# Kernel tuning notes

Measured on AMD Instinct MI355X. Metric: run time of the kernel, lower is better.

## Reference

```python
import jax, jax.numpy as jnp
import numpy as np

D_MODEL = 2048
N_HEADS = 16
HEAD_DIM = D_MODEL // N_HEADS
BATCH = 2
SEQ = 2048


def rotate_half(x):
    x1, x2 = jnp.split(x, 2, axis=-1)
    return jnp.concatenate((-x2, x1), axis=-1)


def rope_emb(seq_len, head_dim, dtype=jnp.float32):
    inv_freq = 1.0 / (10000.0 ** (jnp.arange(0, head_dim, 2, dtype=jnp.float32) / head_dim))
    t = jnp.arange(seq_len, dtype=jnp.float32)
    freqs = jnp.einsum('i,j->ij', t, inv_freq)            # [S, D/2]
    emb = jnp.concatenate((freqs, freqs), axis=-1)        # [S, D]
    return emb[None, :, None, :].astype(dtype)            # [1, S, 1, D]


def apply_rope(x, emb):
    return x * jnp.cos(emb) + rotate_half(x) * jnp.sin(emb)


def setup_inputs() -> dict:
    key = jax.random.key(0)
    ks = jax.random.split(key, 5)
    s = 1.0 / np.sqrt(D_MODEL)
    return {
        'query': jax.random.normal(ks[0], (BATCH, SEQ, D_MODEL), jnp.float32),
        'Wq': jax.random.normal(ks[1], (D_MODEL, D_MODEL), jnp.float32) * s,
        'Wk': jax.random.normal(ks[2], (D_MODEL, D_MODEL), jnp.float32) * s,
        'Wv': jax.random.normal(ks[3], (D_MODEL, D_MODEL), jnp.float32) * s,
        'Wo': jax.random.normal(ks[4], (D_MODEL, D_MODEL), jnp.float32) * s,
    }


def reference(query, Wq, Wk, Wv, Wo):
    B, S, _ = query.shape
    # QKV projections (nn.Linear: x @ W.T), reshape to [B, S, H, Dh]
    q = (query @ Wq.T).reshape(B, S, N_HEADS, HEAD_DIM)
    k = (query @ Wk.T).reshape(B, S, N_HEADS, HEAD_DIM)
    v = (query @ Wv.T).reshape(B, S, N_HEADS, HEAD_DIM)
    emb = rope_emb(S, HEAD_DIM, q.dtype)
    q = apply_rope(q, emb)
    k = apply_rope(k, emb)
    # causal SDPA
    scale = HEAD_DIM ** -0.5
    scores = jnp.einsum('bqhd,bkhd->bhqk', q, k) * scale  # [B, H, S, S]
    causal = jnp.tril(jnp.ones((S, S), dtype=bool))
    scores = jnp.where(causal, scores, jnp.finfo(scores.dtype).min)
    attn = jax.nn.softmax(scores, axis=-1)
    out = jnp.einsum('bhqk,bkhd->bqhd', attn, v).reshape(B, S, D_MODEL)
    return out @ Wo.T
```

## Files before the change

kernel.cpp:

```cpp
#include <hip/hip_runtime.h>
#include <math.h>

#define BATCH 2
#define SEQ 2048
#define DMODEL 2048
#define NHEADS 16
#define HEADDIM 128
#define MTOT (BATCH * SEQ)
#define QKVLD 6144

typedef __attribute__((ext_vector_type(8))) _Float16 half8;
typedef __attribute__((ext_vector_type(4))) _Float16 half4;
typedef __attribute__((ext_vector_type(4))) float f32x4;

__device__ __forceinline__ void gl_lds16(const void* g, void* l) {
    __builtin_amdgcn_global_load_lds(
        (const __attribute__((address_space(1))) unsigned int*)g,
        (__attribute__((address_space(3))) unsigned int*)l, 16, 0, 0);
}

__global__ __launch_bounds__(256) void f2h_multi(const float* __restrict__ query,
                                                 const float* __restrict__ Wq,
                                                 const float* __restrict__ Wk,
                                                 const float* __restrict__ Wv,
                                                 const float* __restrict__ Wo,
                                                 _Float16* __restrict__ xh,
                                                 _Float16* __restrict__ Wh3,
                                                 _Float16* __restrict__ woh) {
    const float* src;
    _Float16* dst;
    size_t i;
    int bx = blockIdx.x;
    if (bx < 4096) {
        src = query; dst = xh;
        i = ((size_t)bx * 256 + threadIdx.x) * 8;
    } else {
        int wi = bx - 4096;
        int y = wi >> 11;
        int off = wi & 2047;
        src = (y == 0) ? Wq : (y == 1) ? Wk : (y == 2) ? Wv : Wo;
        dst = (y == 3) ? woh : Wh3 + (size_t)y * (DMODEL * DMODEL);
        i = ((size_t)off * 256 + threadIdx.x) * 8;
    }
    float4 a = *(const float4*)(src + i);
    float4 b = *(const float4*)(src + i + 4);
    union { uint4 u; _Float16 h[8]; } o;
    o.h[0] = (_Float16)a.x; o.h[1] = (_Float16)a.y;
    o.h[2] = (_Float16)a.z; o.h[3] = (_Float16)a.w;
    o.h[4] = (_Float16)b.x; o.h[5] = (_Float16)b.y;
    o.h[6] = (_Float16)b.z; o.h[7] = (_Float16)b.w;
    *(uint4*)(dst + i) = o.u;
}

__global__ __launch_bounds__(256) void f2h_conv(const float* __restrict__ src,
                                                _Float16* __restrict__ dst) {
    size_t i = ((size_t)blockIdx.x * 256 + threadIdx.x) * 8;
    float4 a = *(const float4*)(src + i);
    float4 b = *(const float4*)(src + i + 4);
    union { uint4 u; _Float16 h[8]; } o;
    o.h[0] = (_Float16)a.x; o.h[1] = (_Float16)a.y;
    o.h[2] = (_Float16)a.z; o.h[3] = (_Float16)a.w;
    o.h[4] = (_Float16)b.x; o.h[5] = (_Float16)b.y;
    o.h[6] = (_Float16)b.z; o.h[7] = (_Float16)b.w;
    *(uint4*)(dst + i) = o.u;
}

#define SB0  __builtin_amdgcn_sched_barrier(0)
#define BAR  __builtin_amdgcn_s_barrier()
#define VMW4 do { SB0; asm volatile("s_waitcnt vmcnt(4)"); SB0; } while (0)
#define VMW0 do { SB0; asm volatile("s_waitcnt vmcnt(0)"); SB0; } while (0)

template <bool F16OUT>
__global__ __launch_bounds__(512, 2) void gemm8p(const _Float16* __restrict__ A,
                                                 const _Float16* __restrict__ W,
                                                 void* __restrict__ Cout,
                                                 int M, int N, int K) {
    __shared__ __align__(16) _Float16 LAb[2][2][128][64];
    __shared__ __align__(16) _Float16 LBb[2][2][128][64];

    const int tid = threadIdx.x;
    const int lane = tid & 63;
    const int wave = tid >> 6;
    const int quad = lane >> 4;
    const int lcol = lane & 15;
    const int wr = wave >> 2;
    const int wc = wave & 3;
    const int m0 = blockIdx.y * 256;
    const int n0 = blockIdx.x * 256;

    const int srow = tid >> 3;
    const int sc8p = tid & 7;
    const int sc8l = sc8p ^ (srow & 7);

#define STA(BUF, HALF, KT)                                                     \
    do {                                                                       \
        _Pragma("unroll") for (int j = 0; j < 2; j++)                          \
            gl_lds16(A + (size_t)(m0 + (HALF)*128 + j*64 + srow) * K +         \
                         (KT)*64 + sc8l*8,                                     \
                     &LAb[BUF][HALF][j*64 + srow][sc8p*8]);                    \
    } while (0)
#define STB(BUF, HALF, KT)                                                     \
    do {                                                                       \
        _Pragma("unroll") for (int j = 0; j < 2; j++)                          \
            gl_lds16(W + (size_t)(n0 + (HALF)*128 + j*64 + srow) * K +         \
                         (KT)*64 + sc8l*8,                                     \
                     &LBb[BUF][HALF][j*64 + srow][sc8p*8]);                    \
    } while (0)

    auto rdA = [&](int buf, int mf, int ks) -> half8 {
        int R = mf * 16 + lcol;
        return *(const half8*)&LAb[buf][wr][R]
                [(ks * 32 + quad * 8) ^ ((lcol & 7) << 3)];
    };
    auto rdB = [&](int buf, int nf, int ks) -> half8 {
        int R = (wc & 1) * 64 + nf * 16 + lcol;
        return *(const half8*)&LBb[buf][wc >> 1][R]
                [(ks * 32 + quad * 8) ^ ((lcol & 7) << 3)];
    };

    f32x4 acc[8][4];
#pragma unroll
    for (int i = 0; i < 8; i++)
#pragma unroll
        for (int j = 0; j < 4; j++) acc[i][j] = (f32x4){0.f, 0.f, 0.f, 0.f};

#define KTILE4(BUF, S1, S2, S3, S4, W4)                                        \
    {                                                                          \
        half8 a[4][2], b[4][2];                                                \
        _Pragma("unroll") for (int mf = 0; mf < 4; mf++)                       \
            _Pragma("unroll") for (int ks = 0; ks < 2; ks++)                   \
                a[mf][ks] = rdA(BUF, mf, ks);                                  \
        _Pragma("unroll") for (int nf = 0; nf < 2; nf++)                       \
            _Pragma("unroll") for (int ks = 0; ks < 2; ks++)                   \
                b[nf][ks] = rdB(BUF, nf, ks);                                  \
        S1; SB0; BAR; SB0;                                                     \
        __builtin_amdgcn_s_setprio(1);                                         \
        _Pragma("unroll") for (int ks = 0; ks < 2; ks++)                       \
            _Pragma("unroll") for (int mf = 0; mf < 4; mf++)                   \
                _Pragma("unroll") for (int nf = 0; nf < 2; nf++)               \
                    acc[mf][nf] = __builtin_amdgcn_mfma_f32_16x16x32_f16(      \
                        a[mf][ks], b[nf][ks], acc[mf][nf], 0, 0, 0);           \
        __builtin_amdgcn_s_setprio(0); SB0; BAR; SB0;                          \
        _Pragma("unroll") for (int nf = 0; nf < 2; nf++)                       \
            _Pragma("unroll") for (int ks = 0; ks < 2; ks++)                   \
                b[2 + nf][ks] = rdB(BUF, 2 + nf, ks);                          \
        S2; SB0; BAR; SB0;                                                     \
        __builtin_amdgcn_s_setprio(1);                                         \
        _Pragma("unroll") for (int ks = 0; ks < 2; ks++)                       \
            _Pragma("unroll") for (int mf = 0; mf < 4; mf++)                   \
                _Pragma("unroll") for (int nf = 0; nf < 2; nf++)               \
                    acc[mf][2 + nf] = __builtin_amdgcn_mfma_f32_16x16x32_f16(  \
                        a[mf][ks], b[2 + nf][ks], acc[mf][2 + nf], 0, 0, 0);   \
        __builtin_amdgcn_s_setprio(0); SB0; BAR; SB0;                          \
        _Pragma("unroll") for (int mf = 0; mf < 4; mf++)                       \
            _Pragma("unroll") for (int ks = 0; ks < 2; ks++)                   \
                a[mf][ks] = rdA(BUF, 4 + mf, ks);                              \
        S3; SB0; BAR; SB0;                                                     \
        __builtin_amdgcn_s_setprio(1);                                         \
        _Pragma("unroll") for (int ks = 0; ks < 2; ks++)                       \
            _Pragma("unroll") for (int mf = 0; mf < 4; mf++)                   \
                _Pragma("unroll") for (int nf = 0; nf < 2; nf++)               \
                    acc[4 + mf][nf] = __builtin_amdgcn_mfma_f32_16x16x32_f16(  \
                        a[mf][ks], b[nf][ks], acc[4 + mf][nf], 0, 0, 0);       \
        __builtin_amdgcn_s_setprio(0); SB0; BAR; SB0;                          \
        S4; W4; BAR; SB0;                                                      \
        __builtin_amdgcn_s_setprio(1);                                         \
        _Pragma("unroll") for (int ks = 0; ks < 2; ks++)                       \
            _Pragma("unroll") for (int mf = 0; mf < 4; mf++)                   \
                _Pragma("unroll") for (int nf = 0; nf < 2; nf++)               \
                    acc[4 + mf][2 + nf] =                                      \
                        __builtin_amdgcn_mfma_f32_16x16x32_f16(                \
                            a[mf][ks], b[2 + nf][ks], acc[4 + mf][2 + nf],     \
                            0, 0, 0);                                          \
        __builtin_amdgcn_s_setprio(0); SB0; BAR; SB0;                          \
    }

    STB(0, 0, 0); STB(0, 1, 0); STA(0, 0, 0); STA(0, 1, 0);
    STB(1, 0, 1); STB(1, 1, 1);
    VMW4; BAR; SB0;

    const int niter = K >> 7;
    for (int i = 0; i < niter - 1; ++i) {
        const int t0 = 2 * i;
        KTILE4(0, STA(1, 0, t0 + 1), STA(1, 1, t0 + 1),
                  STB(0, 0, t0 + 2), STB(0, 1, t0 + 2), VMW4);
        KTILE4(1, STA(0, 0, t0 + 2), STA(0, 1, t0 + 2),
                  STB(1, 0, t0 + 3), STB(1, 1, t0 + 3), VMW4);
    }
    {
        const int t0 = 2 * (niter - 1);
        KTILE4(0, STA(1, 0, t0 + 1), STA(1, 1, t0 + 1),
                  (void)0, (void)0, VMW0);
        KTILE4(1, (void)0, (void)0, (void)0, (void)0, (void)0);
    }

    float* Cf = (float*)Cout;
    _Float16* Ch = (_Float16*)Cout;
#pragma unroll
    for (int mf = 0; mf < 8; mf++)
#pragma unroll
        for (int nf = 0; nf < 4; nf++)
#pragma unroll
            for (int r = 0; r < 4; r++) {
                size_t row = m0 + wr * 128 + mf * 16 + quad * 4 + r;
                size_t col = n0 + wc * 64 + nf * 16 + lcol;
                if (F16OUT)
                    Ch[row * N + col] = (_Float16)acc[mf][nf][r];
                else
                    Cf[row * N + col] = acc[mf][nf][r];
            }
#undef KTILE4
#undef STA
#undef STB
}

template <bool F16OUT>
__global__ __launch_bounds__(256) void gemm_h(const _Float16* __restrict__ A,
                                              const _Float16* __restrict__ W,
                                              void* __restrict__ Cout,
                                              int M, int N, int K) {
    __shared__ __align__(16) _Float16 As[128 * 32];
    __shared__ __align__(16) _Float16 Bs[128 * 32];

    const int tid = threadIdx.x;
    const int wv = tid >> 6;
    const int ln = tid & 63;
    const int quad = ln >> 4;
    const int lcol = ln & 15;
    const int m0 = blockIdx.y * 128;
    const int n0 = blockIdx.x * 128;
    const int wm = (wv >> 1) * 64;
    const int wn = (wv & 1) * 64;

    const int srow = ln >> 2;
    const int kblk = (ln & 3) * 8;

    f32x4 acc[4][4];
#pragma unroll
    for (int i = 0; i < 4; i++)
#pragma unroll
        for (int j = 0; j < 4; j++) acc[i][j] = (f32x4){0.f, 0.f, 0.f, 0.f};

    for (int k0 = 0; k0 < K; k0 += 32) {
        __syncthreads();
#pragma unroll
        for (int j = 0; j < 2; j++) {
            int r = wv * 32 + j * 16 + srow;
            gl_lds16(A + (size_t)(m0 + r) * K + k0 + kblk, &As[r * 32 + kblk]);
            gl_lds16(W + (size_t)(n0 + r) * K + k0 + kblk, &Bs[r * 32 + kblk]);
        }
        __syncthreads();

        half8 af[4], bf[4];
#pragma unroll
        for (int ms = 0; ms < 4; ms++)
            af[ms] = *(const half8*)&As[(wm + ms * 16 + lcol) * 32 + quad * 8];
#pragma unroll
        for (int ns = 0; ns < 4; ns++)
            bf[ns] = *(const half8*)&Bs[(wn + ns * 16 + lcol) * 32 + quad * 8];
#pragma unroll
        for (int ms = 0; ms < 4; ms++)
#pragma unroll
            for (int ns = 0; ns < 4; ns++)
                acc[ms][ns] = __builtin_amdgcn_mfma_f32_16x16x32_f16(
                    af[ms], bf[ns], acc[ms][ns], 0, 0, 0);
    }

    float* Cf = (float*)Cout;
    _Float16* Ch = (_Float16*)Cout;
#pragma unroll
    for (int ms = 0; ms < 4; ms++)
#pragma unroll
        for (int ns = 0; ns < 4; ns++)
#pragma unroll
            for (int r = 0; r < 4; r++) {
                size_t row = m0 + wm + ms * 16 + quad * 4 + r;
                size_t col = n0 + wn + ns * 16 + lcol;
                if (F16OUT)
                    Ch[row * N + col] = (_Float16)acc[ms][ns][r];
                else
                    Cf[row * N + col] = acc[ms][ns][r];
            }
}

__global__ __launch_bounds__(256) void prep_kv(_Float16* __restrict__ qkv,
                                               _Float16* __restrict__ vtb) {
    __shared__ __align__(16) _Float16 T[32][72];
    int bx = blockIdx.x;
    const int tid = threadIdx.x;

    if (bx < 4096) {
        size_t idx = (size_t)bx * 256 + tid;
        int chunk = (int)(idx & 7);
        int h = (int)((idx >> 3) & (NHEADS - 1));
        int qk = (int)((idx >> 7) & 1);
        int m = (int)(idx >> 8);
        int s = m & (SEQ - 1);
        float scale = qk ? 1.0f : 0.08838834764831845f;
        int d8 = chunk * 8;

        size_t base = (size_t)m * QKVLD + qk * DMODEL + h * HEADDIM + d8;
        union { uint4 u; _Float16 hh[8]; } u0, u1, o0, o1;
        u0.u = *(const uint4*)(qkv + base);
        u1.u = *(const uint4*)(qkv + base + 64);
#pragma unroll
        for (int j = 0; j < 8; j++) {
            float inv = __expf(-(float)(d8 + j) * 0.14391156831212787f);
            float f = (float)s * inv;
            float sn, cs;
            __sincosf(f, &sn, &cs);
            float x1 = (float)u0.hh[j];
            float x2 = (float)u1.hh[j];
            o0.hh[j] = (_Float16)((x1 * cs - x2 * sn) * scale);
            o1.hh[j] = (_Float16)((x2 * cs + x1 * sn) * scale);
        }
        *(uint4*)(qkv + base) = o0.u;
        *(uint4*)(qkv + base + 64) = o1.u;
    } else {
        int v = bx - 4096;
        const int s0 = (v & 31) * 64;
        const int d0 = ((v >> 5) & 3) * 32;
        const int bh = v >> 7;
        const int b = bh >> 4;
        const int h = bh & 15;

        {
            int s = tid >> 2;
            int d8 = (tid & 3) * 8;
            union { uint4 u; _Float16 hh[8]; } vv;
            vv.u = *(const uint4*)(qkv + (size_t)(b * SEQ + s0 + s) * QKVLD +
                                   2 * DMODEL + h * HEADDIM + d0 + d8);
#pragma unroll
            for (int j = 0; j < 8; j++) T[d8 + j][s] = vv.hh[j];
        }
        __syncthreads();

        int row = tid >> 3;
        int chunk = tid & 7;
        uint4 val = *(const uint4*)&T[row][chunk * 8];
        *(uint4*)(vtb + ((size_t)(bh * HEADDIM + d0 + row)) * SEQ + s0 + chunk * 8) = val;
    }
}

__global__ __launch_bounds__(512) void attn_mfma(const _Float16* __restrict__ qkv,
                                                 const _Float16* __restrict__ vtb,
                                                 _Float16* __restrict__ ab) {
    __shared__ __align__(16) _Float16 Ks[64][136];
    __shared__ __align__(16) _Float16 Vts[128][72];
    __shared__ __align__(16) _Float16 Ps[8][16][72];

    const int tid = threadIdx.x;
    const int wave = tid >> 6;
    const int lane = tid & 63;
    const int quad = lane >> 4;
    const int lcol = lane & 15;

    const int h = blockIdx.y;
    const int b = blockIdx.z;
    const int qtA = blockIdx.x;

    const int wtile = (wave < 4) ? qtA : (15 - qtA);
    const int q0w = wtile * 128 + (wave & 3) * 32;
    const int nkt = 2 * (15 - qtA) + 2;

    const int kr0 = tid >> 4;
    const int ko0 = (tid & 15) * 8;
    const int vr0 = tid >> 3;
    const int vo0 = (tid & 7) * 8;

    const _Float16* kbp = qkv + (size_t)b * SEQ * QKVLD + DMODEL + h * HEADDIM;
    const _Float16* vbp = vtb + ((size_t)(b * NHEADS + h) * HEADDIM) * SEQ;

    uint4 kA, kB, vA, vB;
#define ISSUE_LOAD(kb)                                                        \
    do {                                                                      \
        int _kb = (kb);                                                       \
        kA = *(const uint4*)(kbp + (size_t)(_kb + kr0) * QKVLD + ko0);        \
        kB = *(const uint4*)(kbp + (size_t)(_kb + 32 + kr0) * QKVLD + ko0);   \
        vA = *(const uint4*)(vbp + (size_t)vr0 * SEQ + _kb + vo0);            \
        vB = *(const uint4*)(vbp + (size_t)(vr0 + 64) * SEQ + _kb + vo0);     \
    } while (0)

    ISSUE_LOAD(0);

    half8 aq0[4], aq1[4];
    {
        const _Float16* q0p = qkv + (size_t)(b * SEQ + q0w + lcol) * QKVLD + h * HEADDIM;
        const _Float16* q1p = q0p + (size_t)16 * QKVLD;
#pragma unroll
        for (int st = 0; st < 4; st++) {
            aq0[st] = *(const half8*)(q0p + quad * 8 + 32 * st);
            aq1[st] = *(const half8*)(q1p + quad * 8 + 32 * st);
        }
    }

    f32x4 Of0[8], Of1[8];
#pragma unroll
    for (int dt = 0; dt < 8; dt++) {
        Of0[dt] = (f32x4){0.f, 0.f, 0.f, 0.f};
        Of1[dt] = (f32x4){0.f, 0.f, 0.f, 0.f};
    }
    float m_s0 = -1e30f, l_s0 = 0.f;
    float m_s1 = -1e30f, l_s1 = 0.f;

    for (int kt = 0; kt < nkt; ++kt) {
        const int kbase = kt << 6;

        __syncthreads();
        *(uint4*)&Ks[kr0][ko0]        = kA;
        *(uint4*)&Ks[kr0 + 32][ko0]   = kB;
        *(uint4*)&Vts[vr0][vo0]       = vA;
        *(uint4*)&Vts[vr0 + 64][vo0]  = vB;
        __syncthreads();

        if (kt + 1 < nkt) ISSUE_LOAD((kt + 1) << 6);

        if (kbase > q0w + 31) continue;

        f32x4 Sc0[4], Sc1[4];
#pragma unroll
        for (int s = 0; s < 4; s++) {
            Sc0[s] = (f32x4){0.f, 0.f, 0.f, 0.f};
            Sc1[s] = (f32x4){0.f, 0.f, 0.f, 0.f};
#pragma unroll
            for (int st = 0; st < 4; st++) {
                half8 bk = *(const half8*)&Ks[16 * s + lcol][quad * 8 + 32 * st];
                Sc0[s] = __builtin_amdgcn_mfma_f32_16x16x32_f16(bk, aq0[st], Sc0[s], 0, 0, 0);
                Sc1[s] = __builtin_amdgcn_mfma_f32_16x16x32_f16(bk, aq1[st], Sc1[s], 0, 0, 0);
            }
        }

        if (kbase + 63 > q0w) {
#pragma unroll
            for (int s = 0; s < 4; s++)
#pragma unroll
                for (int r = 0; r < 4; r++) {
                    int kk = kbase + 16 * s + quad * 4 + r;
                    if (kk > q0w + lcol)      Sc0[s][r] = -1e30f;
                    if (kk > q0w + 16 + lcol) Sc1[s][r] = -1e30f;
                }
        }

        half8 ap0[2], ap1[2];

        {
            float pmax = Sc0[0][0];
#pragma unroll
            for (int s = 0; s < 4; s++)
#pragma unroll
                for (int r = 0; r < 4; r++) pmax = fmaxf(pmax, Sc0[s][r]);
            pmax = fmaxf(pmax, __shfl_xor(pmax, 16));
            pmax = fmaxf(pmax, __shfl_xor(pmax, 32));
            if (!__all(pmax <= m_s0 + 5.0f)) {
                float mnew = fmaxf(m_s0, pmax);
                float alpha = __expf(m_s0 - mnew);
                m_s0 = mnew;
                l_s0 *= alpha;
                float a0 = __shfl(alpha, quad * 4 + 0);
                float a1 = __shfl(alpha, quad * 4 + 1);
                float a2 = __shfl(alpha, quad * 4 + 2);
                float a3 = __shfl(alpha, quad * 4 + 3);
#pragma unroll
                for (int dt = 0; dt < 8; dt++) {
                    Of0[dt][0] *= a0; Of0[dt][1] *= a1;
                    Of0[dt][2] *= a2; Of0[dt][3] *= a3;
                }
            }
            float sum = 0.f;
#pragma unroll
            for (int s = 0; s < 4; s++)
#pragma unroll
                for (int r = 0; r < 4; r++) {
                    float p = __expf(Sc0[s][r] - m_s0);
                    Sc0[s][r] = p;
                    sum += p;
                }
            sum += __shfl_xor(sum, 16);
            sum += __shfl_xor(sum, 32);
            l_s0 += sum;
#pragma unroll
            for (int s = 0; s < 4; s++) {
                half4 pk;
                pk[0] = (_Float16)Sc0[s][0]; pk[1] = (_Float16)Sc0[s][1];
                pk[2] = (_Float16)Sc0[s][2]; pk[3] = (_Float16)Sc0[s][3];
                *(half4*)&Ps[wave][lcol][16 * s + 4 * quad] = pk;
            }
            ap0[0] = *(const half8*)&Ps[wave][lcol][quad * 8];
            ap0[1] = *(const half8*)&Ps[wave][lcol][quad * 8 + 32];
        }

        {
            float pmax = Sc1[0][0];
#pragma unroll
            for (int s = 0; s < 4; s++)
#pragma unroll
                for (int r = 0; r < 4; r++) pmax = fmaxf(pmax, Sc1[s][r]);
            pmax = fmaxf(pmax, __shfl_xor(pmax, 16));
            pmax = fmaxf(pmax, __shfl_xor(pmax, 32));
            if (!__all(pmax <= m_s1 + 5.0f)) {
                float mnew = fmaxf(m_s1, pmax);
                float alpha = __expf(m_s1 - mnew);
                m_s1 = mnew;
                l_s1 *= alpha;
                float a0 = __shfl(alpha, quad * 4 + 0);
                float a1 = __shfl(alpha, quad * 4 + 1);
                float a2 = __shfl(alpha, quad * 4 + 2);
                float a3 = __shfl(alpha, quad * 4 + 3);
#pragma unroll
                for (int dt = 0; dt < 8; dt++) {
                    Of1[dt][0] *= a0; Of1[dt][1] *= a1;
                    Of1[dt][2] *= a2; Of1[dt][3] *= a3;
                }
            }
            float sum = 0.f;
#pragma unroll
            for (int s = 0; s < 4; s++)
#pragma unroll
                for (int r = 0; r < 4; r++) {
                    float p = __expf(Sc1[s][r] - m_s1);
                    Sc1[s][r] = p;
                    sum += p;
                }
            sum += __shfl_xor(sum, 16);
            sum += __shfl_xor(sum, 32);
            l_s1 += sum;
#pragma unroll
            for (int s = 0; s < 4; s++) {
                half4 pk;
                pk[0] = (_Float16)Sc1[s][0]; pk[1] = (_Float16)Sc1[s][1];
                pk[2] = (_Float16)Sc1[s][2]; pk[3] = (_Float16)Sc1[s][3];
                *(half4*)&Ps[wave][lcol][16 * s + 4 * quad] = pk;
            }
            ap1[0] = *(const half8*)&Ps[wave][lcol][quad * 8];
            ap1[1] = *(const half8*)&Ps[wave][lcol][quad * 8 + 32];
        }

#pragma unroll
        for (int dt = 0; dt < 8; dt++) {
#pragma unroll
            for (int st = 0; st < 2; st++) {
                half8 bv = *(const half8*)&Vts[16 * dt + lcol][quad * 8 + 32 * st];
                Of0[dt] = __builtin_amdgcn_mfma_f32_16x16x32_f16(
                    st == 0 ? ap0[0] : ap0[1], bv, Of0[dt], 0, 0, 0);
                Of1[dt] = __builtin_amdgcn_mfma_f32_16x16x32_f16(
                    st == 0 ? ap1[0] : ap1[1], bv, Of1[dt], 0, 0, 0);
            }
        }
    }

    {
        float invl = 1.f / l_s0;
        float i0 = __shfl(invl, quad * 4 + 0);
        float i1 = __shfl(invl, quad * 4 + 1);
        float i2 = __shfl(invl, quad * 4 + 2);
        float i3 = __shfl(invl, quad * 4 + 3);
        _Float16* obase =
            ab + (size_t)(b * SEQ + q0w + quad * 4) * DMODEL + h * HEADDIM;
#pragma unroll
        for (int dt = 0; dt < 8; dt++) {
            obase[(size_t)0 * DMODEL + 16 * dt + lcol] = (_Float16)(Of0[dt][0] * i0);
            obase[(size_t)1 * DMODEL + 16 * dt + lcol] = (_Float16)(Of0[dt][1] * i1);
            obase[(size_t)2 * DMODEL + 16 * dt + lcol] = (_Float16)(Of0[dt][2] * i2);
            obase[(size_t)3 * DMODEL + 16 * dt + lcol] = (_Float16)(Of0[dt][3] * i3);
        }
    }
    {
        float invl = 1.f / l_s1;
        float i0 = __shfl(invl, quad * 4 + 0);
        float i1 = __shfl(invl, quad * 4 + 1);
        float i2 = __shfl(invl, quad * 4 + 2);
        float i3 = __shfl(invl, quad * 4 + 3);
        _Float16* obase =
            ab + (size_t)(b * SEQ + q0w + 16 + quad * 4) * DMODEL + h * HEADDIM;
#pragma unroll
        for (int dt = 0; dt < 8; dt++) {
            obase[(size_t)0 * DMODEL + 16 * dt + lcol] = (_Float16)(Of1[dt][0] * i0);
            obase[(size_t)1 * DMODEL + 16 * dt + lcol] = (_Float16)(Of1[dt][1] * i1);
            obase[(size_t)2 * DMODEL + 16 * dt + lcol] = (_Float16)(Of1[dt][2] * i2);
            obase[(size_t)3 * DMODEL + 16 * dt + lcol] = (_Float16)(Of1[dt][3] * i3);
        }
    }
#undef ISSUE_LOAD
}

extern "C" void kernel_launch(void* const* d_in, const int* in_sizes, int n_in,
                              void* d_out, int out_size, void* d_ws, size_t ws_size,
                              hipStream_t stream) {
    const float* query = (const float*)d_in[0];
    const float* Wq = (const float*)d_in[1];
    const float* Wk = (const float*)d_in[2];
    const float* Wv = (const float*)d_in[3];
    const float* Wo = (const float*)d_in[4];
    float* out = (float*)d_out;

    const size_t MB = 1024 * 1024;
    char* w = (char*)d_ws;
    _Float16* xh   = (_Float16*)(w + 0 * MB);
    _Float16* ab   = (_Float16*)(w + 0 * MB);
    _Float16* qkvh = (_Float16*)(w + 16 * MB);
    _Float16* Wh3  = (_Float16*)(w + 64 * MB);
    _Float16* vtb  = (_Float16*)(w + 88 * MB);
    _Float16* woh  = (_Float16*)(w + 104 * MB);

    const int convW = (DMODEL * DMODEL) / (256 * 8);
    const bool fuseWo = ws_size >= (size_t)112 * MB;

    int convBlocks = 4096 + (fuseWo ? 4 : 3) * 2048;
    f2h_multi<<<convBlocks, 256, 0, stream>>>(query, Wq, Wk, Wv, Wo, xh, Wh3, woh);

    gemm8p<true><<<dim3(QKVLD / 256, MTOT / 256), 512, 0, stream>>>(
        xh, Wh3, qkvh, MTOT, QKVLD, DMODEL);

    prep_kv<<<4096 + 4096, 256, 0, stream>>>(qkvh, vtb);

    attn_mfma<<<dim3(8, NHEADS, BATCH), 512, 0, stream>>>(qkvh, vtb, ab);

    const _Float16* woSrc;
    if (fuseWo) {
        woSrc = woh;
    } else {
        f2h_conv<<<convW, 256, 0, stream>>>(Wo, Wh3);
        woSrc = Wh3;
    }
    gemm_h<false><<<dim3(DMODEL / 128, MTOT / 128), 256, 0, stream>>>(
        ab, woSrc, out, MTOT, DMODEL, DMODEL);
}
```

Before: 406.1 us.

## Fuse RoPE, Q scaling and V transpose into QKV GEMM epilogue

```diff
diff --git a/kernel.cpp b/kernel.cpp
--- a/kernel.cpp
+++ b/kernel.cpp
@@ -70,14 +70,15 @@
 #define VMW4 do { SB0; asm volatile("s_waitcnt vmcnt(4)"); SB0; } while (0)
 #define VMW0 do { SB0; asm volatile("s_waitcnt vmcnt(0)"); SB0; } while (0)
 
-template <bool F16OUT>
-__global__ __launch_bounds__(512, 2) void gemm8p(const _Float16* __restrict__ A,
-                                                 const _Float16* __restrict__ W,
-                                                 void* __restrict__ Cout,
-                                                 int M, int N, int K) {
-    __shared__ __align__(16) _Float16 LAb[2][2][128][64];
-    __shared__ __align__(16) _Float16 LBb[2][2][128][64];
-
+__global__ __launch_bounds__(512, 2) void gemm_qkv(const _Float16* __restrict__ A,
+                                                   const _Float16* __restrict__ W,
+                                                   _Float16* __restrict__ qkv,
+                                                   _Float16* __restrict__ vtb) {
+    __shared__ __align__(16) char lds_raw[131072];
+    _Float16 (*LAb)[2][128][64] = (_Float16(*)[2][128][64])lds_raw;
+    _Float16 (*LBb)[2][128][64] = (_Float16(*)[2][128][64])(lds_raw + 65536);
+
+    const int K = DMODEL;
     const int tid = threadIdx.x;
     const int lane = tid & 63;
     const int wave = tid >> 6;
@@ -194,21 +195,69 @@
         KTILE4(1, (void)0, (void)0, (void)0, (void)0, (void)0);
     }
 
-    float* Cf = (float*)Cout;
-    _Float16* Ch = (_Float16*)Cout;
-#pragma unroll
-    for (int mf = 0; mf < 8; mf++)
-#pragma unroll
-        for (int nf = 0; nf < 4; nf++)
-#pragma unroll
-            for (int r = 0; r < 4; r++) {
-                size_t row = m0 + wr * 128 + mf * 16 + quad * 4 + r;
-                size_t col = n0 + wc * 64 + nf * 16 + lcol;
-                if (F16OUT)
-                    Ch[row * N + col] = (_Float16)acc[mf][nf][r];
-                else
-                    Cf[row * N + col] = acc[mf][nf][r];
-            }
+    if (n0 < 2 * DMODEL) {
+        const float scale = (n0 < DMODEL) ? 0.08838834764831845f : 1.0f;
+        _Float16 (*T)[256] = (_Float16(*)[256])lds_raw;
+
+        __syncthreads();
+#pragma unroll
+        for (int mf = 0; mf < 8; mf++)
+#pragma unroll
+            for (int nf = 0; nf < 4; nf++)
+#pragma unroll
+                for (int r = 0; r < 4; r++)
+                    T[wr * 128 + mf * 16 + quad * 4 + r]
+                     [wc * 64 + nf * 16 + lcol] = (_Float16)acc[mf][nf][r];
+        __syncthreads();
+
+#pragma unroll
+        for (int u = 0; u < 8; ++u) {
+            int unit = tid + 512 * u;
+            int row = unit >> 4;
+            int hh = (unit >> 3) & 1;
+            int c8 = (unit & 7) * 8;
+            int s = (m0 + row) & (SEQ - 1);
+            int cb = hh * 128 + c8;
+            half8 x1v = *(const half8*)&T[row][cb];
+            half8 x2v = *(const half8*)&T[row][cb + 64];
+            half8 o1v, o2v;
+#pragma unroll
+            for (int j = 0; j < 8; j++) {
+                float inv = __expf(-(float)(c8 + j) * 0.14391156831212787f);
+                float f = (float)s * inv;
+                float sn, cs;
+                __sincosf(f, &sn, &cs);
+                float x1 = (float)x1v[j];
+                float x2 = (float)x2v[j];
+                o1v[j] = (_Float16)((x1 * cs - x2 * sn) * scale);
+                o2v[j] = (_Float16)((x2 * cs + x1 * sn) * scale);
+            }
+            _Float16* g = qkv + (size_t)(m0 + row) * QKVLD + n0 + cb;
+            *(half8*)g = o1v;
+            *(half8*)(g + 64) = o2v;
+        }
+    } else {
+        const int vbase = n0 - 2 * DMODEL;
+#pragma unroll
+        for (int mf = 0; mf < 8; mf++) {
+            int m = m0 + wr * 128 + mf * 16 + quad * 4;
+            int b = m >> 11;
+            int s = m & (SEQ - 1);
+#pragma unroll
+            for (int nf = 0; nf < 4; nf++) {
+                int col = vbase + wc * 64 + nf * 16 + lcol;
+                int hh = col >> 7;
+                int d = col & 127;
+                half4 pk;
+                pk[0] = (_Float16)acc[mf][nf][0];
+                pk[1] = (_Float16)acc[mf][nf][1];
+                pk[2] = (_Float16)acc[mf][nf][2];
+                pk[3] = (_Float16)acc[mf][nf][3];
+                *(half4*)(vtb +
+                          ((size_t)((b * NHEADS + hh) * HEADDIM + d)) * SEQ + s) = pk;
+            }
+        }
+    }
 #undef KTILE4
 #undef STA
 #undef STB
@@ -281,65 +330,6 @@
                 else
                     Cf[row * N + col] = acc[ms][ns][r];
             }
-}
-
-__global__ __launch_bounds__(256) void prep_kv(_Float16* __restrict__ qkv,
-                                               _Float16* __restrict__ vtb) {
-    __shared__ __align__(16) _Float16 T[32][72];
-    int bx = blockIdx.x;
-    const int tid = threadIdx.x;
-
-    if (bx < 4096) {
-        size_t idx = (size_t)bx * 256 + tid;
-        int chunk = (int)(idx & 7);
-        int h = (int)((idx >> 3) & (NHEADS - 1));
-        int qk = (int)((idx >> 7) & 1);
-        int m = (int)(idx >> 8);
-        int s = m & (SEQ - 1);
-        float scale = qk ? 1.0f : 0.08838834764831845f;
-        int d8 = chunk * 8;
-
-        size_t base = (size_t)m * QKVLD + qk * DMODEL + h * HEADDIM + d8;
-        union { uint4 u; _Float16 hh[8]; } u0, u1, o0, o1;
-        u0.u = *(const uint4*)(qkv + base);
-        u1.u = *(const uint4*)(qkv + base + 64);
-#pragma unroll
-        for (int j = 0; j < 8; j++) {
-            float inv = __expf(-(float)(d8 + j) * 0.14391156831212787f);
-            float f = (float)s * inv;
-            float sn, cs;
-            __sincosf(f, &sn, &cs);
-            float x1 = (float)u0.hh[j];
-            float x2 = (float)u1.hh[j];
-            o0.hh[j] = (_Float16)((x1 * cs - x2 * sn) * scale);
-            o1.hh[j] = (_Float16)((x2 * cs + x1 * sn) * scale);
-        }
-        *(uint4*)(qkv + base) = o0.u;
-        *(uint4*)(qkv + base + 64) = o1.u;
-    } else {
-        int v = bx - 4096;
-        const int s0 = (v & 31) * 64;
-        const int d0 = ((v >> 5) & 3) * 32;
-        const int bh = v >> 7;
-        const int b = bh >> 4;
-        const int h = bh & 15;
-
-        {
-            int s = tid >> 2;
-            int d8 = (tid & 3) * 8;
-            union { uint4 u; _Float16 hh[8]; } vv;
-            vv.u = *(const uint4*)(qkv + (size_t)(b * SEQ + s0 + s) * QKVLD +
-                                   2 * DMODEL + h * HEADDIM + d0 + d8);
-#pragma unroll
-            for (int j = 0; j < 8; j++) T[d8 + j][s] = vv.hh[j];
-        }
-        __syncthreads();
-
-        int row = tid >> 3;
-        int chunk = tid & 7;
-        uint4 val = *(const uint4*)&T[row][chunk * 8];
-        *(uint4*)(vtb + ((size_t)(bh * HEADDIM + d0 + row)) * SEQ + s0 + chunk * 8) = val;
-    }
 }
 
 __global__ __launch_bounds__(512) void attn_mfma(const _Float16* __restrict__ qkv,
@@ -608,10 +598,7 @@
     int convBlocks = 4096 + (fuseWo ? 4 : 3) * 2048;
     f2h_multi<<<convBlocks, 256, 0, stream>>>(query, Wq, Wk, Wv, Wo, xh, Wh3, woh);
 
-    gemm8p<true><<<dim3(QKVLD / 256, MTOT / 256), 512, 0, stream>>>(
-        xh, Wh3, qkvh, MTOT, QKVLD, DMODEL);
-
-    prep_kv<<<4096 + 4096, 256, 0, stream>>>(qkvh, vtb);
+    gemm_qkv<<<dim3(QKVLD / 256, MTOT / 256), 512, 0, stream>>>(xh, Wh3, qkvh, vtb);
 
     attn_mfma<<<dim3(8, NHEADS, BATCH), 512, 0, stream>>>(qkvh, vtb, ab);
 
```

Measured after the change: 384.1 us. 5.4% less time.
